# Optimization experiments

Measured on AMD Instinct MI355X. Metric: run time of the kernel, lower is better.

Reference implementation:

```python
import jax, jax.numpy as jnp
import numpy as np

T, B, NMUL = 730, 1000, 8
NEARZERO = 1e-5
LENF = 15
A_LO, A_HI = 0.1, 1.0
B_LO, B_HI = 50.0, 500.0
C_LO, C_HI = 0.0, 1.0
D_LO, D_HI = 0.01, 0.9
RA_LO, RA_HI = 0.0, 2.9
RB_LO, RB_HI = 0.0, 6.5
S_INIT, G_INIT = 50.0, 10.0


def setup_inputs() -> dict:
    key = jax.random.key(0)
    k1, k2 = jax.random.split(key)
    # forcing: prcp in [0,10) mm/day, pet in [0,5) mm/day
    x = jax.random.uniform(k1, (T, B, 2), dtype=jnp.float32) * jnp.array([10.0, 5.0], dtype=jnp.float32)
    # NN-produced raw params in [0,1): 4*NMUL physical + 2 routing
    raw_phy_static = jax.random.uniform(k2, (B, 4 * NMUL + 2), dtype=jnp.float32)
    return {"x": x, "raw_phy_static": raw_phy_static}


def _descale(p, lo, hi):
    return p * (hi - lo) + lo


def _uh_gamma(rout_a, rout_b):
    # gamma-distribution unit hydrograph, (B,) params -> (B, LENF) kernel
    aa = jax.nn.relu(rout_a)[:, None] + 0.1      # shape parameter
    theta = jax.nn.relu(rout_b)[:, None] + 0.5   # scale parameter
    t = jnp.arange(0.5, LENF, 1.0, dtype=jnp.float32)[None, :]  # midpoints 0.5..14.5
    logw = (aa - 1.0) * jnp.log(t) - t / theta - jax.scipy.special.gammaln(aa) - aa * jnp.log(theta)
    w = jnp.exp(logw)
    return w / w.sum(1, keepdims=True)


def _uh_conv(q, UH):
    # causal per-basin convolution: y[b,t] = sum_k q[b,t-k]*UH[b,k]; q (B,T), UH (B,LENF)
    n = q.shape[1]
    conv1 = lambda qb, wb: jnp.convolve(qb, wb, mode='full')[:n]
    return jax.vmap(conv1)(q, UH)


def reference(x, raw_phy_static):
    phy = raw_phy_static[:, :4 * NMUL].reshape(B, 4, NMUL)  # (B,4,NMUL)
    a = _descale(phy[:, 0], A_LO, A_HI)
    b = _descale(phy[:, 1], B_LO, B_HI)
    c = _descale(phy[:, 2], C_LO, C_HI)
    d = _descale(phy[:, 3], D_LO, D_HI)
    rout_a = _descale(raw_phy_static[:, 4 * NMUL], RA_LO, RA_HI)  # (B,)
    rout_b = _descale(raw_phy_static[:, 4 * NMUL + 1], RB_LO, RB_HI)

    ones_mul = jnp.ones((1, 1, NMUL), dtype=x.dtype)
    P = x[:, :, 0:1] * ones_mul    # (T,B,NMUL)
    PET = x[:, :, 1:2] * ones_mul  # (T,B,NMUL)

    S0 = jnp.full((B, NMUL), S_INIT, dtype=x.dtype)
    G0 = jnp.full((B, NMUL), G_INIT, dtype=x.dtype)

    def step(carry, inp):
        S, G = carry
        p, pet = inp
        W = p + S                                   # available water
        term = (W + b) / (2.0 * a)
        Y = term - jnp.sqrt(jnp.maximum(term * term - W * b / a, NEARZERO))  # ET opportunity
        S_new = Y * jnp.exp(-pet / b)               # soil storage
        AET = Y - S_new                             # actual ET
        avail = W - Y                               # water available for runoff/recharge
        Qsurf = (1.0 - c) * avail                   # direct runoff
        G_new = (G + c * avail) / (1.0 + d)         # groundwater storage
        Qgw = d * G_new                             # baseflow
        Qsim = Qsurf + Qgw
        return (S_new, G_new), (Qsim, Qsurf, Qgw, AET, S_new, G_new, W, Y)

    (_, _), (Qsim, Qsurf, Qgw, AET, Sout, Gout, Wout, Yout) = jax.lax.scan(step, (S0, G0), (P, PET))

    UH = _uh_gamma(rout_a, rout_b)                  # (B,LENF)
    Qs = _uh_conv(Qsim.mean(-1).T, UH).T[..., None]        # routed streamflow (T,B,1)
    Qsurf_r = _uh_conv(Qsurf.mean(-1).T, UH).T[..., None]  # routed surface runoff
    Qgw_r = _uh_conv(Qgw.mean(-1).T, UH).T[..., None]      # routed groundwater flow

    out = jnp.concatenate([
        Qs, Qsurf_r, Qgw_r,
        AET.mean(-1, keepdims=True),
        Sout.mean(-1, keepdims=True),
        Gout.mean(-1, keepdims=True),
    ], axis=-1)  # (T,B,6)
    return out
```

## Files before the change

kernel.cpp:

```cpp
#include <hip/hip_runtime.h>
#include <math.h>

#define T_STEPS 730
#define NB      1000
#define LENF    15
#define NEARZ   1e-5f
#define SGW     8000
#define TT      50
#define BBLK    32

#define STEPA(CURV)                                                            \
  {                                                                            \
    float pcp = (CURV).x, pet = (CURV).y;                                      \
    float W     = pcp + S;                                                     \
    float term  = fmaf(W, inv2a, pb2a);                                        \
    float disc  = fmaf(term, term, -(W * boa));                                \
    float r     = __builtin_amdgcn_sqrtf(fmaxf(disc, NEARZ));                  \
    float Y     = term - r;                                                    \
    float e     = __builtin_amdgcn_exp2f(pet * nbl);                           \
    float Sn    = Y * e;                                                       \
    float avail = W - Y;                                                       \
    float Gn    = fmaf(pc, avail, G) * i1d;                                    \
    S = Sn; G = Gn;                                                            \
    *psg = make_float2(Sn, Gn);                                                \
    psg += SGW;                                                                \
  }

#define PREFETCH(BUF, CI)                                                      \
  _Pragma("unroll")                                                            \
  for (int j = 0; j < 8; ++j) {                                                \
      BUF[j] = xs[((CI) * 8 + j) * 8 + bl];                                    \
  }                                                                            \
  __builtin_amdgcn_sched_barrier(0);

__global__ __launch_bounds__(64, 1) void scan_state(const float* __restrict__ x,
                                                    const float* __restrict__ raw,
                                                    float2* __restrict__ sg) {
    __shared__ float4 xs4[2944];
    const float2* xs = (const float2*)xs4;

    const int L   = threadIdx.x;
    const int gid = blockIdx.x * 64 + L;
    const int b   = gid >> 3;
    const int m   = gid & 7;
    const int bl  = L >> 3;

    {
        float4 tmp[46];
#pragma unroll
        for (int ch = 0; ch < 46; ++ch) {
            int idx = ch * 64 + L;
            int row = idx >> 2;
            row = row < T_STEPS ? row : (T_STEPS - 1);
            tmp[ch] = *(const float4*)((const char*)x + (size_t)row * (NB * 8)
                                       + (size_t)(blockIdx.x * 64)
                                       + (size_t)(idx & 3) * 16);
        }
#pragma unroll
        for (int ch = 0; ch < 46; ++ch) xs4[ch * 64 + L] = tmp[ch];
    }
    __syncthreads();

    const float* rp = raw + b * 34;
    float pa = rp[0 * 8 + m] * 0.9f + 0.1f;
    float pb = rp[1 * 8 + m] * 450.0f + 50.0f;
    float pc = rp[2 * 8 + m];
    float pd = rp[3 * 8 + m] * 0.89f + 0.01f;

    float inv2a = 1.0f / (2.0f * pa);
    float pb2a  = pb * inv2a;
    float boa   = pb / pa;
    float nbl   = -1.4426950408889634f / pb;
    float i1d   = 1.0f / (1.0f + pd);

    float S = 50.0f, G = 10.0f;
    float2* psg = sg + gid;

    float2 A[8], Bb[8], Cc[8];
    PREFETCH(A, 0)
    PREFETCH(Bb, 1)

    for (int g = 0; g < 15; ++g) {
        const int c0 = 6 * g;
        PREFETCH(Cc, c0 + 2)
#pragma unroll
        for (int j = 0; j < 8; ++j) STEPA(A[j])
        PREFETCH(A, c0 + 3)
#pragma unroll
        for (int j = 0; j < 8; ++j) STEPA(Bb[j])
        PREFETCH(Bb, c0 + 4)
#pragma unroll
        for (int j = 0; j < 8; ++j) STEPA(Cc[j])
        PREFETCH(Cc, c0 + 5)
#pragma unroll
        for (int j = 0; j < 8; ++j) STEPA(A[j])
        PREFETCH(A, c0 + 6)
#pragma unroll
        for (int j = 0; j < 8; ++j) STEPA(Bb[j])
        PREFETCH(Bb, c0 + 7)
#pragma unroll
        for (int j = 0; j < 8; ++j) STEPA(Cc[j])
    }
#pragma unroll
    for (int j = 0; j < 8; ++j) STEPA(A[j])
    STEPA(Bb[0])
    STEPA(Bb[1])
}

template <int CTRL>
__device__ __forceinline__ float dpp_mov(float x) {
    int xi = __builtin_bit_cast(int, x);
    int r  = __builtin_amdgcn_update_dpp(0, xi, CTRL, 0xF, 0xF, true);
    return __builtin_bit_cast(float, r);
}
__device__ __forceinline__ float sum8(float v) {
    v += dpp_mov<0xB1>(v);
    v += dpp_mov<0x4E>(v);
    v += dpp_mov<0x141>(v);
    return v;
}

__global__ __launch_bounds__(256) void finalize(const float* __restrict__ x,
                                                const float* __restrict__ raw,
                                                const float2* __restrict__ sg,
                                                float* __restrict__ out) {
    __shared__ float qsh[TT + 14][BBLK + 1];
    __shared__ float qgh[TT + 14][BBLK + 1];

    const int tid   = threadIdx.x;
    const int lb    = tid >> 3;
    const int m     = tid & 7;
    const int tbase = blockIdx.x * TT;
    const int b0    = blockIdx.y * BBLK;
    const int b     = b0 + lb;
    const bool bval = b < NB;
    const int bc    = bval ? b : (NB - 1);
    const int lane  = bc * 8 + m;

    const float* rp = raw + bc * 34;
    float pbm = rp[8 + m] * 450.0f + 50.0f;
    float e2s = 1.4426950408889634f / pbm;
    float omc = 1.0f - rp[16 + m];
    float dm  = rp[24 + m] * 0.89f + 0.01f;

    const float2* __restrict__ xf = (const float2*)x;

    float2 sgb[4], pvb[4];
#pragma unroll
    for (int d = 0; d < 4; ++d) {
        int tt = tbase + d - 14;
        int tc = tt < 0 ? 0 : (tt >= T_STEPS ? T_STEPS - 1 : tt);
        sgb[d] = sg[(size_t)tc * SGW + lane];
        pvb[d] = xf[tc * NB + bc];
    }
    float Sprev = (tbase > 0) ? sg[(size_t)(tbase - 15) * SGW + lane].x : 50.0f;

    for (int rr = 0; rr < TT + 14; rr += 4) {
#pragma unroll
        for (int d = 0; d < 4; ++d) {
            const int r  = rr + d;
            const int tt = tbase + r - 14;
            float2 sgv = sgb[d];
            float2 pv  = pvb[d];
            {
                int tn = tt + 4;
                int tc = tn < 0 ? 0 : (tn >= T_STEPS ? T_STEPS - 1 : tn);
                sgb[d] = sg[(size_t)tc * SGW + lane];
                pvb[d] = xf[tc * NB + bc];
            }
            const bool tval = (tt >= 0) && (tt < T_STEPS);
            float qs = 0.0f, qg = 0.0f, aet = 0.0f, sX = 0.0f, gX = 0.0f;
            if (tval) {
                float sp    = (tt == 0) ? 50.0f : Sprev;
                float y     = sgv.x * __builtin_amdgcn_exp2f(pv.y * e2s);
                float avail = (pv.x + sp) - y;
                qs  = omc * avail;
                qg  = dm * sgv.y;
                aet = y - sgv.x;
                sX  = sgv.x;
                gX  = sgv.y;
            }
            qs = sum8(qs);
            qg = sum8(qg);
            if (m == 0) { qsh[r][lb] = qs; qgh[r][lb] = qg; }
            if (r >= 14 && tval) {
                float a_s = sum8(aet);
                float s_s = sum8(sX);
                float g_s = sum8(gX);
                if (bval && m < 3) {
                    float v = (m == 0) ? a_s : ((m == 1) ? s_s : g_s);
                    out[((size_t)tt * NB + b) * 6 + 3 + m] = v * 0.125f;
                }
            }
            Sprev = sgv.x;
        }
    }
    __syncthreads();

    const int bl2 = tid & 31;
    const int tl0 = tid >> 5;
    const int b2  = b0 + bl2;
    if (b2 >= NB) return;

    const float* rp2 = raw + b2 * 34;
    float ra = rp2[32] * 2.9f;
    float rb = rp2[33] * 6.5f;
    float aa = fmaxf(ra, 0.0f) + 0.1f;
    float th = fmaxf(rb, 0.0f) + 0.5f;
    float inv_th = 1.0f / th;
    float am1 = aa - 1.0f;
    float w[LENF];
    float sw = 0.0f;
#pragma unroll
    for (int k = 0; k < LENF; ++k) {
        float tk = (float)k + 0.5f;
        w[k] = __expf(am1 * __logf(tk) - tk * inv_th);
        sw += w[k];
    }
    float invs = 0.125f / sw;
#pragma unroll
    for (int k = 0; k < LENF; ++k) w[k] *= invs;

#pragma unroll
    for (int it = 0; it < 7; ++it) {
        int tl = tl0 + it * 8;
        int t  = tbase + tl;
        if (tl < TT && t < T_STEPS) {
            float ys = 0.0f, yg = 0.0f;
#pragma unroll
            for (int k = 0; k < LENF; ++k) {
                ys = fmaf(qsh[tl + 14 - k][bl2], w[k], ys);
                yg = fmaf(qgh[tl + 14 - k][bl2], w[k], yg);
            }
            float* o = out + ((size_t)t * NB + b2) * 6;
            o[0] = ys + yg;
            o[1] = ys;
            o[2] = yg;
        }
    }
}

#define STEPF(CURV)                                                            \
  {                                                                            \
    float pcp = (CURV).x, pet = (CURV).y;                                      \
    float W     = pcp + S;                                                     \
    float term  = fmaf(W, inv2a, pb2a);                                        \
    float disc  = fmaf(term, term, -(W * boa));                                \
    float r     = __builtin_amdgcn_sqrtf(fmaxf(disc, NEARZ));                  \
    float Y     = term - r;                                                    \
    float e     = __builtin_amdgcn_exp2f(pet * ninvbl2);                       \
    float Sn    = Y * e;                                                       \
    float AET   = Y - Sn;                                                      \
    float avail = W - Y;                                                       \
    float Qs    = omc * avail;                                                 \
    float Gn    = fmaf(pc, avail, G) * inv1pd;                                 \
    float Qg    = pd * Gn;                                                     \
    S = Sn; G = Gn;                                                            \
    float qs_s = sum8(Qs);                                                     \
    float qg_s = sum8(Qg);                                                     \
    float ae_s = sum8(AET);                                                    \
    float s_s  = sum8(Sn);                                                     \
    float g_s  = sum8(Gn);                                                     \
    float v = qs_s;                                                            \
    v = (m == 1) ? qg_s : v;                                                   \
    v = (m == 2) ? ae_s : v;                                                   \
    v = (m == 3) ? s_s  : v;                                                   \
    v = (m >= 4) ? g_s  : v;                                                   \
    *optr = v * 0.125f;                                                        \
    optr += incr;                                                              \
  }

__global__ __launch_bounds__(64, 1) void scan_fb(const float* __restrict__ x,
                                                 const float* __restrict__ raw,
                                                 float* __restrict__ out,
                                                 float* __restrict__ qs_ws,
                                                 float* __restrict__ qg_ws,
                                                 float* __restrict__ dummy) {
    const int L  = threadIdx.x;
    const int lb = L >> 3;
    const int m  = L & 7;
    const int b  = blockIdx.x * 8 + lb;

    const float* rp = raw + b * 34;
    float pa = rp[0 * 8 + m] * 0.9f + 0.1f;
    float pb = rp[1 * 8 + m] * 450.0f + 50.0f;
    float pc = rp[2 * 8 + m];
    float pd = rp[3 * 8 + m] * 0.89f + 0.01f;
    float inv2a   = 1.0f / (2.0f * pa);
    float pb2a    = pb * inv2a;
    float boa     = pb / pa;
    float ninvbl2 = -1.4426950408889634f / pb;
    float omc     = 1.0f - pc;
    float inv1pd  = 1.0f / (1.0f + pd);

    float* optr;
    long long incr;
    if      (m == 0) { optr = qs_ws + b;                      incr = NB;     }
    else if (m == 1) { optr = qg_ws + b;                      incr = NB;     }
    else if (m <= 4) { optr = out + (long long)b * 6 + m + 1; incr = NB * 6; }
    else             { optr = dummy + (blockIdx.x * 64 + L);  incr = 0;      }

    float S = 50.0f, G = 10.0f;
    const float2* __restrict__ xf = (const float2*)x;

    float2 A[10], B[10], C[10];
#pragma unroll
    for (int j = 0; j < 10; ++j) A[j] = xf[j * NB + b];
#pragma unroll
    for (int j = 0; j < 10; ++j) B[j] = xf[(10 + j) * NB + b];

    for (int cg = 0; cg < 24; ++cg) {
        const int c0 = 3 * cg;
#pragma unroll
        for (int j = 0; j < 10; ++j) C[j] = xf[((c0 + 2) * 10 + j) * NB + b];
        __builtin_amdgcn_sched_barrier(0);
#pragma unroll
        for (int j = 0; j < 10; ++j) STEPF(A[j]);
#pragma unroll
        for (int j = 0; j < 10; ++j) A[j] = xf[((c0 + 3) * 10 + j) * NB + b];
        __builtin_amdgcn_sched_barrier(0);
#pragma unroll
        for (int j = 0; j < 10; ++j) STEPF(B[j]);
#pragma unroll
        for (int j = 0; j < 10; ++j) {
            int t = (c0 + 4) * 10 + j;
            t = t < T_STEPS ? t : (T_STEPS - 1);
            B[j] = xf[t * NB + b];
        }
        __builtin_amdgcn_sched_barrier(0);
#pragma unroll
        for (int j = 0; j < 10; ++j) STEPF(C[j]);
    }
#pragma unroll
    for (int j = 0; j < 10; ++j) STEPF(A[j]);
}

__global__ __launch_bounds__(256) void uh_fb(const float* __restrict__ raw,
                                             float* __restrict__ uh) {
    int b = blockIdx.x * 256 + threadIdx.x;
    if (b >= NB) return;
    float ra = raw[b * 34 + 32] * 2.9f;
    float rb = raw[b * 34 + 33] * 6.5f;
    float aa = fmaxf(ra, 0.0f) + 0.1f;
    float th = fmaxf(rb, 0.0f) + 0.5f;
    float inv_th = 1.0f / th;
    float am1 = aa - 1.0f;
    float w[LENF];
    float s = 0.0f;
#pragma unroll
    for (int k = 0; k < LENF; ++k) {
        float t = (float)k + 0.5f;
        w[k] = __expf(am1 * __logf(t) - t * inv_th);
        s += w[k];
    }
    float invs = 1.0f / s;
#pragma unroll
    for (int k = 0; k < LENF; ++k) uh[k * NB + b] = w[k] * invs;
}

__global__ __launch_bounds__(256) void conv_fb(const float* __restrict__ qs_ws,
                                               const float* __restrict__ qg_ws,
                                               const float* __restrict__ uh,
                                               float* __restrict__ out) {
    int b = blockIdx.x * 256 + threadIdx.x;
    int t = blockIdx.y;
    if (b >= NB) return;
    float ys = 0.0f, yg = 0.0f;
    int kmax = t < (LENF - 1) ? t : (LENF - 1);
    for (int k = 0; k <= kmax; ++k) {
        float w = uh[k * NB + b];
        ys = fmaf(qs_ws[(t - k) * NB + b], w, ys);
        yg = fmaf(qg_ws[(t - k) * NB + b], w, yg);
    }
    float* o = out + (t * NB + b) * 6;
    o[0] = ys + yg;
    o[1] = ys;
    o[2] = yg;
}

extern "C" void kernel_launch(void* const* d_in, const int* in_sizes, int n_in,
                              void* d_out, int out_size, void* d_ws, size_t ws_size,
                              hipStream_t stream) {
    const float* x   = (const float*)d_in[0];
    const float* raw = (const float*)d_in[1];
    float* out = (float*)d_out;

    const size_t need = (size_t)T_STEPS * SGW * sizeof(float2);
    if (ws_size >= need) {
        float2* sg = (float2*)d_ws;
        scan_state<<<dim3(SGW / 64), dim3(64),  0, stream>>>(x, raw, sg);
        finalize  <<<dim3((T_STEPS + TT - 1) / TT, (NB + BBLK - 1) / BBLK),
                     dim3(256), 0, stream>>>(x, raw, sg, out);
    } else {
        float* qs = (float*)d_ws;
        float* qg = qs + (size_t)T_STEPS * NB;
        float* uh = qg + (size_t)T_STEPS * NB;
        float* dm = uh + (size_t)LENF * NB;
        uh_fb  <<<dim3((NB + 255) / 256),          dim3(256), 0, stream>>>(raw, uh);
        scan_fb<<<dim3(NB / 8),                    dim3(64),  0, stream>>>(x, raw, out, qs, qg, dm);
        conv_fb<<<dim3((NB + 255) / 256, T_STEPS), dim3(256), 0, stream>>>(qs, qg, uh, out);
    }
}
```

Measured before the change: 113.6 us.

## Fuse member-mean reductions into scan and split routing into separate UH and conv kernels

The scan kernel now computes Qsurf, Qgw, AET, S and G in place and reduces them across the 8 multipliers with DPP lane shuffles. It writes the per-basin mean flows and state outputs directly, so the full per-member S/G state is no longer written to the workspace and re-read. A small kernel builds the unit hydrograph, and a separate conv kernel does the causal convolution from the reduced (T,B) flow buffer. This cuts workspace traffic roughly eightfold. In exchange, the latency-bound serial scan carries five DPP reductions and strided global stores per step, and it adds a third kernel launch.

```diff
diff --git a/kernel.cpp b/kernel.cpp
--- a/kernel.cpp
+++ b/kernel.cpp
@@ -6,24 +6,44 @@
 #define LENF    15
 #define NEARZ   1e-5f
 #define SGW     8000
-#define TT      50
-#define BBLK    32
-
-#define STEPA(CURV)                                                            \
-  {                                                                            \
-    float pcp = (CURV).x, pet = (CURV).y;                                      \
-    float W     = pcp + S;                                                     \
-    float term  = fmaf(W, inv2a, pb2a);                                        \
-    float disc  = fmaf(term, term, -(W * boa));                                \
-    float r     = __builtin_amdgcn_sqrtf(fmaxf(disc, NEARZ));                  \
-    float Y     = term - r;                                                    \
-    float e     = __builtin_amdgcn_exp2f(pet * nbl);                           \
-    float Sn    = Y * e;                                                       \
-    float avail = W - Y;                                                       \
-    float Gn    = fmaf(pc, avail, G) * i1d;                                    \
-    S = Sn; G = Gn;                                                            \
-    *psg = make_float2(Sn, Gn);                                                \
-    psg += SGW;                                                                \
+
+template <int CTRL>
+__device__ __forceinline__ float dpp_mov(float x) {
+    int xi = __builtin_bit_cast(int, x);
+    int r  = __builtin_amdgcn_update_dpp(0, xi, CTRL, 0xF, 0xF, true);
+    return __builtin_bit_cast(float, r);
+}
+__device__ __forceinline__ float sum8(float v) {
+    v += dpp_mov<0xB1>(v);
+    v += dpp_mov<0x4E>(v);
+    v += dpp_mov<0x141>(v);
+    return v;
+}
+
+#define STEPC(CURV)                                                           \
+  {                                                                           \
+    float pcp = (CURV).x, pet = (CURV).y;                                     \
+    float W     = pcp + S;                                                    \
+    float term  = fmaf(W, inv2a, pb2a);                                       \
+    float disc  = fmaf(term, term, -(W * boa));                               \
+    float r     = __builtin_amdgcn_sqrtf(fmaxf(disc, NEARZ));                 \
+    float Y     = term - r;                                                   \
+    float e     = __builtin_amdgcn_exp2f(pet * nbl);                          \
+    float Sn    = Y * e;                                                      \
+    float avail = W - Y;                                                      \
+    float Gn    = fmaf(pc, avail, G) * i1d;                                   \
+    float Qs    = omc * avail;                                                \
+    float Qg    = pd * Gn;                                                    \
+    S = Sn; G = Gn;                                                           \
+    float qs_s = sum8(Qs);                                                    \
+    float qg_s = sum8(Qg);                                                    \
+    float y_s  = sum8(Y);                                                     \
+    float s_s  = sum8(Sn);                                                    \
+    float g_s  = sum8(Gn);                                                    \
+    if (m == 3) *qp = make_float2(qs_s, qg_s);                                \
+    float ov = (m == 0) ? (y_s - s_s) : ((m == 1) ? s_s : g_s);               \
+    if (m < 3) *optr = ov * 0.125f;                                           \
+    qp += NB; optr += NB * 6;                                                 \
   }
 
 #define PREFETCH(BUF, CI)                                                      \
@@ -33,9 +53,10 @@
   }                                                                            \
   __builtin_amdgcn_sched_barrier(0);
 
-__global__ __launch_bounds__(64, 1) void scan_state(const float* __restrict__ x,
+__global__ __launch_bounds__(64, 1) void scan_fused(const float* __restrict__ x,
                                                     const float* __restrict__ raw,
-                                                    float2* __restrict__ sg) {
+                                                    float2* __restrict__ qsg,
+                                                    float* __restrict__ out) {
     __shared__ float4 xs4[2944];
     const float2* xs = (const float2*)xs4;
 
@@ -72,9 +93,11 @@
     float boa   = pb / pa;
     float nbl   = -1.4426950408889634f / pb;
     float i1d   = 1.0f / (1.0f + pd);
+    float omc   = 1.0f - pc;
 
     float S = 50.0f, G = 10.0f;
-    float2* psg = sg + gid;
+    float2* qp   = qsg + b;
+    float*  optr = out + (size_t)b * 6 + 3 + (m < 3 ? m : 0);
 
     float2 A[8], Bb[8], Cc[8];
     PREFETCH(A, 0)
@@ -84,160 +107,69 @@
         const int c0 = 6 * g;
         PREFETCH(Cc, c0 + 2)
 #pragma unroll
-        for (int j = 0; j < 8; ++j) STEPA(A[j])
+        for (int j = 0; j < 8; ++j) STEPC(A[j])
         PREFETCH(A, c0 + 3)
 #pragma unroll
-        for (int j = 0; j < 8; ++j) STEPA(Bb[j])
+        for (int j = 0; j < 8; ++j) STEPC(Bb[j])
         PREFETCH(Bb, c0 + 4)
 #pragma unroll
-        for (int j = 0; j < 8; ++j) STEPA(Cc[j])
+        for (int j = 0; j < 8; ++j) STEPC(Cc[j])
         PREFETCH(Cc, c0 + 5)
 #pragma unroll
-        for (int j = 0; j < 8; ++j) STEPA(A[j])
+        for (int j = 0; j < 8; ++j) STEPC(A[j])
         PREFETCH(A, c0 + 6)
 #pragma unroll
-        for (int j = 0; j < 8; ++j) STEPA(Bb[j])
+        for (int j = 0; j < 8; ++j) STEPC(Bb[j])
         PREFETCH(Bb, c0 + 7)
 #pragma unroll
-        for (int j = 0; j < 8; ++j) STEPA(Cc[j])
-    }
-#pragma unroll
-    for (int j = 0; j < 8; ++j) STEPA(A[j])
-    STEPA(Bb[0])
-    STEPA(Bb[1])
-}
-
-template <int CTRL>
-__device__ __forceinline__ float dpp_mov(float x) {
-    int xi = __builtin_bit_cast(int, x);
-    int r  = __builtin_amdgcn_update_dpp(0, xi, CTRL, 0xF, 0xF, true);
-    return __builtin_bit_cast(float, r);
-}
-__device__ __forceinline__ float sum8(float v) {
-    v += dpp_mov<0xB1>(v);
-    v += dpp_mov<0x4E>(v);
-    v += dpp_mov<0x141>(v);
-    return v;
-}
-
-__global__ __launch_bounds__(256) void finalize(const float* __restrict__ x,
-                                                const float* __restrict__ raw,
-                                                const float2* __restrict__ sg,
-                                                float* __restrict__ out) {
-    __shared__ float qsh[TT + 14][BBLK + 1];
-    __shared__ float qgh[TT + 14][BBLK + 1];
-
-    const int tid   = threadIdx.x;
-    const int lb    = tid >> 3;
-    const int m     = tid & 7;
-    const int tbase = blockIdx.x * TT;
-    const int b0    = blockIdx.y * BBLK;
-    const int b     = b0 + lb;
-    const bool bval = b < NB;
-    const int bc    = bval ? b : (NB - 1);
-    const int lane  = bc * 8 + m;
-
-    const float* rp = raw + bc * 34;
-    float pbm = rp[8 + m] * 450.0f + 50.0f;
-    float e2s = 1.4426950408889634f / pbm;
-    float omc = 1.0f - rp[16 + m];
-    float dm  = rp[24 + m] * 0.89f + 0.01f;
-
-    const float2* __restrict__ xf = (const float2*)x;
-
-    float2 sgb[4], pvb[4];
-#pragma unroll
-    for (int d = 0; d < 4; ++d) {
-        int tt = tbase + d - 14;
-        int tc = tt < 0 ? 0 : (tt >= T_STEPS ? T_STEPS - 1 : tt);
-        sgb[d] = sg[(size_t)tc * SGW + lane];
-        pvb[d] = xf[tc * NB + bc];
-    }
-    float Sprev = (tbase > 0) ? sg[(size_t)(tbase - 15) * SGW + lane].x : 50.0f;
-
-    for (int rr = 0; rr < TT + 14; rr += 4) {
-#pragma unroll
-        for (int d = 0; d < 4; ++d) {
-            const int r  = rr + d;
-            const int tt = tbase + r - 14;
-            float2 sgv = sgb[d];
-            float2 pv  = pvb[d];
-            {
-                int tn = tt + 4;
-                int tc = tn < 0 ? 0 : (tn >= T_STEPS ? T_STEPS - 1 : tn);
-                sgb[d] = sg[(size_t)tc * SGW + lane];
-                pvb[d] = xf[tc * NB + bc];
-            }
-            const bool tval = (tt >= 0) && (tt < T_STEPS);
-            float qs = 0.0f, qg = 0.0f, aet = 0.0f, sX = 0.0f, gX = 0.0f;
-            if (tval) {
-                float sp    = (tt == 0) ? 50.0f : Sprev;
-                float y     = sgv.x * __builtin_amdgcn_exp2f(pv.y * e2s);
-                float avail = (pv.x + sp) - y;
-                qs  = omc * avail;
-                qg  = dm * sgv.y;
-                aet = y - sgv.x;
-                sX  = sgv.x;
-                gX  = sgv.y;
-            }
-            qs = sum8(qs);
-            qg = sum8(qg);
-            if (m == 0) { qsh[r][lb] = qs; qgh[r][lb] = qg; }
-            if (r >= 14 && tval) {
-                float a_s = sum8(aet);
-                float s_s = sum8(sX);
-                float g_s = sum8(gX);
-                if (bval && m < 3) {
-                    float v = (m == 0) ? a_s : ((m == 1) ? s_s : g_s);
-                    out[((size_t)tt * NB + b) * 6 + 3 + m] = v * 0.125f;
-                }
-            }
-            Sprev = sgv.x;
-        }
-    }
-    __syncthreads();
-
-    const int bl2 = tid & 31;
-    const int tl0 = tid >> 5;
-    const int b2  = b0 + bl2;
-    if (b2 >= NB) return;
-
-    const float* rp2 = raw + b2 * 34;
-    float ra = rp2[32] * 2.9f;
-    float rb = rp2[33] * 6.5f;
+        for (int j = 0; j < 8; ++j) STEPC(Cc[j])
+    }
+#pragma unroll
+    for (int j = 0; j < 8; ++j) STEPC(A[j])
+    STEPC(Bb[0])
+    STEPC(Bb[1])
+}
+
+__global__ __launch_bounds__(256) void uh_k(const float* __restrict__ raw,
+                                            float* __restrict__ uh) {
+    int b = blockIdx.x * 256 + threadIdx.x;
+    if (b >= NB) return;
+    float ra = raw[b * 34 + 32] * 2.9f;
+    float rb = raw[b * 34 + 33] * 6.5f;
     float aa = fmaxf(ra, 0.0f) + 0.1f;
     float th = fmaxf(rb, 0.0f) + 0.5f;
     float inv_th = 1.0f / th;
     float am1 = aa - 1.0f;
     float w[LENF];
-    float sw = 0.0f;
+    float s = 0.0f;
 #pragma unroll
     for (int k = 0; k < LENF; ++k) {
-        float tk = (float)k + 0.5f;
-        w[k] = __expf(am1 * __logf(tk) - tk * inv_th);
-        sw += w[k];
-    }
-    float invs = 0.125f / sw;
-#pragma unroll
-    for (int k = 0; k < LENF; ++k) w[k] *= invs;
-
-#pragma unroll
-    for (int it = 0; it < 7; ++it) {
-        int tl = tl0 + it * 8;
-        int t  = tbase + tl;
-        if (tl < TT && t < T_STEPS) {
-            float ys = 0.0f, yg = 0.0f;
-#pragma unroll
-            for (int k = 0; k < LENF; ++k) {
-                ys = fmaf(qsh[tl + 14 - k][bl2], w[k], ys);
-                yg = fmaf(qgh[tl + 14 - k][bl2], w[k], yg);
-            }
-            float* o = out + ((size_t)t * NB + b2) * 6;
-            o[0] = ys + yg;
-            o[1] = ys;
-            o[2] = yg;
-        }
-    }
+        float t = (float)k + 0.5f;
+        w[k] = __expf(am1 * __logf(t) - t * inv_th);
+        s += w[k];
+    }
+    float invs = 0.125f / s;
+#pragma unroll
+    for (int k = 0; k < LENF; ++k) uh[k * NB + b] = w[k] * invs;
+}
+
+__global__ __launch_bounds__(256) void conv2(const float2* __restrict__ qsg,
+                                             const float* __restrict__ uh,
+                                             float* __restrict__ out) {
+    int b = blockIdx.x * 256 + threadIdx.x;
+    int t = blockIdx.y;
+    if (b >= NB) return;
+    float ys = 0.0f, yg = 0.0f;
+    int kmax = t < (LENF - 1) ? t : (LENF - 1);
+    for (int k = 0; k <= kmax; ++k) {
+        float w  = uh[k * NB + b];
+        float2 q = qsg[(size_t)(t - k) * NB + b];
+        ys = fmaf(q.x, w, ys);
+        yg = fmaf(q.y, w, yg);
+    }
+    float* o = out + ((size_t)t * NB + b) * 6;
+    *(float2*)o = make_float2(ys + yg, ys);
+    o[2] = yg;
 }
 
 #define STEPF(CURV)                                                            \
@@ -385,12 +317,14 @@
     const float* raw = (const float*)d_in[1];
     float* out = (float*)d_out;
 
-    const size_t need = (size_t)T_STEPS * SGW * sizeof(float2);
+    const size_t need = (size_t)T_STEPS * NB * sizeof(float2)
+                      + (size_t)LENF * NB * sizeof(float);
     if (ws_size >= need) {
-        float2* sg = (float2*)d_ws;
-        scan_state<<<dim3(SGW / 64), dim3(64),  0, stream>>>(x, raw, sg);
-        finalize  <<<dim3((T_STEPS + TT - 1) / TT, (NB + BBLK - 1) / BBLK),
-                     dim3(256), 0, stream>>>(x, raw, sg, out);
+        float2* qsg = (float2*)d_ws;
+        float*  uh  = (float*)(qsg + (size_t)T_STEPS * NB);
+        uh_k      <<<dim3((NB + 255) / 256), dim3(256), 0, stream>>>(raw, uh);
+        scan_fused<<<dim3(SGW / 64),         dim3(64),  0, stream>>>(x, raw, qsg, out);
+        conv2     <<<dim3((NB + 255) / 256, T_STEPS), dim3(256), 0, stream>>>(qsg, uh, out);
     } else {
         float* qs = (float*)d_ws;
         float* qg = qs + (size_t)T_STEPS * NB;
```

New measurement: 216.3 us. 1.9x slower.

## Store only S per step with sparse G checkpoints, recompute G in finalize

Applied to the files above, without the earlier changes.

The scan kernel now writes only the soil storage S for each step, packing two steps per float2, and writes groundwater G only at checkpoints spaced one finalize tile apart. The finalize kernel reloads G from the checkpoint and recomputes the G recurrence across its tile, including the 14-step halo. The time tile grows from 50 to 64 to match the checkpoint spacing. This roughly halves workspace write and read traffic in exchange for a serial G recurrence in finalize and extra per-step bookkeeping in the scan.

```diff
diff --git a/kernel.cpp b/kernel.cpp
--- a/kernel.cpp
+++ b/kernel.cpp
@@ -6,10 +6,26 @@
 #define LENF    15
 #define NEARZ   1e-5f
 #define SGW     8000
-#define TT      50
+#define TT      64
 #define BBLK    32
-
-#define STEPA(CURV)                                                            \
+#define NPAIR   365
+#define NCHK    11
+
+
+template <int CTRL>
+__device__ __forceinline__ float dpp_mov(float x) {
+    int xi = __builtin_bit_cast(int, x);
+    int r  = __builtin_amdgcn_update_dpp(0, xi, CTRL, 0xF, 0xF, true);
+    return __builtin_bit_cast(float, r);
+}
+__device__ __forceinline__ float sum8(float v) {
+    v += dpp_mov<0xB1>(v);
+    v += dpp_mov<0x4E>(v);
+    v += dpp_mov<0x141>(v);
+    return v;
+}
+
+#define STEPA(CURV, TB, J)                                                     \
   {                                                                            \
     float pcp = (CURV).x, pet = (CURV).y;                                      \
     float W     = pcp + S;                                                     \
@@ -22,8 +38,9 @@
     float avail = W - Y;                                                       \
     float Gn    = fmaf(pc, avail, G) * i1d;                                    \
     S = Sn; G = Gn;                                                            \
-    *psg = make_float2(Sn, Gn);                                                \
-    psg += SGW;                                                                \
+    if (((J) & 1) == 0) Skeep = Sn;                                            \
+    else { *ps2 = make_float2(Skeep, Sn); ps2 += SGW; }                        \
+    if ((TB) + (J) == nextchk) { *gc = Gn; gc += SGW; nextchk += TT; }         \
   }
 
 #define PREFETCH(BUF, CI)                                                      \
@@ -35,7 +52,8 @@
 
 __global__ __launch_bounds__(64, 1) void scan_state(const float* __restrict__ x,
                                                     const float* __restrict__ raw,
-                                                    float2* __restrict__ sg) {
+                                                    float2* __restrict__ sp,
+                                                    float* __restrict__ gchk) {
     __shared__ float4 xs4[2944];
     const float2* xs = (const float2*)xs4;
 
@@ -73,8 +91,10 @@
     float nbl   = -1.4426950408889634f / pb;
     float i1d   = 1.0f / (1.0f + pd);
 
-    float S = 50.0f, G = 10.0f;
-    float2* psg = sg + gid;
+    float S = 50.0f, G = 10.0f, Skeep = 0.0f;
+    float2* ps2 = sp + gid;
+    float*  gc  = gchk + gid;
+    int nextchk = TT - 15;
 
     float2 A[8], Bb[8], Cc[8];
     PREFETCH(A, 0)
@@ -82,47 +102,76 @@
 
     for (int g = 0; g < 15; ++g) {
         const int c0 = 6 * g;
+        const int t0 = 48 * g;
         PREFETCH(Cc, c0 + 2)
 #pragma unroll
-        for (int j = 0; j < 8; ++j) STEPA(A[j])
+        for (int j = 0; j < 8; ++j) STEPA(A[j],  t0,      j)
         PREFETCH(A, c0 + 3)
 #pragma unroll
-        for (int j = 0; j < 8; ++j) STEPA(Bb[j])
+        for (int j = 0; j < 8; ++j) STEPA(Bb[j], t0 + 8,  j)
         PREFETCH(Bb, c0 + 4)
 #pragma unroll
-        for (int j = 0; j < 8; ++j) STEPA(Cc[j])
+        for (int j = 0; j < 8; ++j) STEPA(Cc[j], t0 + 16, j)
         PREFETCH(Cc, c0 + 5)
 #pragma unroll
-        for (int j = 0; j < 8; ++j) STEPA(A[j])
+        for (int j = 0; j < 8; ++j) STEPA(A[j],  t0 + 24, j)
         PREFETCH(A, c0 + 6)
 #pragma unroll
-        for (int j = 0; j < 8; ++j) STEPA(Bb[j])
+        for (int j = 0; j < 8; ++j) STEPA(Bb[j], t0 + 32, j)
         PREFETCH(Bb, c0 + 7)
 #pragma unroll
-        for (int j = 0; j < 8; ++j) STEPA(Cc[j])
-    }
-#pragma unroll
-    for (int j = 0; j < 8; ++j) STEPA(A[j])
-    STEPA(Bb[0])
-    STEPA(Bb[1])
-}
-
-template <int CTRL>
-__device__ __forceinline__ float dpp_mov(float x) {
-    int xi = __builtin_bit_cast(int, x);
-    int r  = __builtin_amdgcn_update_dpp(0, xi, CTRL, 0xF, 0xF, true);
-    return __builtin_bit_cast(float, r);
-}
-__device__ __forceinline__ float sum8(float v) {
-    v += dpp_mov<0xB1>(v);
-    v += dpp_mov<0x4E>(v);
-    v += dpp_mov<0x141>(v);
-    return v;
-}
+        for (int j = 0; j < 8; ++j) STEPA(Cc[j], t0 + 40, j)
+    }
+#pragma unroll
+    for (int j = 0; j < 8; ++j) STEPA(A[j], 720, j)
+    STEPA(Bb[0], 728, 0)
+    STEPA(Bb[1], 728, 1)
+}
+
+#define ROW(SN, XV, TTE, RE)                                                   \
+  {                                                                            \
+    const int tt = (TTE); const int r = (RE);                                  \
+    const bool tval = (tt >= 0) && (tt < T_STEPS);                             \
+    float qs = 0.f, qg = 0.f, aet = 0.f, sX = 0.f, gX = 0.f;                   \
+    if (tval) {                                                                \
+      float sn  = (SN);                                                        \
+      float spv = (tt == 0) ? 50.0f : Sprev;                                   \
+      float y   = sn * __builtin_amdgcn_exp2f((XV).y * e2s);                   \
+      float avail = ((XV).x + spv) - y;                                        \
+      G = fmaf(pc, avail, G) * i1d;                                            \
+      qs = omc * avail; qg = pd * G; aet = y - sn; sX = sn; gX = G;            \
+      Sprev = sn;                                                              \
+    }                                                                          \
+    qs = sum8(qs); qg = sum8(qg);                                              \
+    if (m == 0) { qsh[r][lb] = qs; qgh[r][lb] = qg; }                          \
+    if (r >= 14 && tval) {                                                     \
+      float a_s = sum8(aet), s_s = sum8(sX), g_s = sum8(gX);                   \
+      if (bval && m < 3) {                                                     \
+        float v = (m == 0) ? a_s : ((m == 1) ? s_s : g_s);                     \
+        out[((size_t)tt * NB + b) * 6 + 3 + m] = v * 0.125f;                   \
+      }                                                                        \
+    }                                                                          \
+  }
+
+#define PAIRSTEP(PH)                                                           \
+  {                                                                            \
+    const int pidx = g2 * 3 + (PH);                                            \
+    const int tt0  = tbase - 14 + 2 * pidx;                                    \
+    float2 sv  = sb[PH];                                                       \
+    float2 xv0 = x0b[PH];                                                      \
+    float2 xv1 = x1b[PH];                                                      \
+    { int tp = tt0 + 6; tp = tp < 0 ? 0 : (tp > 728 ? 728 : tp);               \
+      sb[PH]  = sp[(size_t)(tp >> 1) * SGW + lane];                            \
+      x0b[PH] = xf[tp * NB + bc];                                              \
+      x1b[PH] = xf[(tp + 1) * NB + bc]; }                                      \
+    ROW(sv.x, xv0, tt0,     2 * pidx)                                          \
+    ROW(sv.y, xv1, tt0 + 1, 2 * pidx + 1)                                      \
+  }
 
 __global__ __launch_bounds__(256) void finalize(const float* __restrict__ x,
                                                 const float* __restrict__ raw,
-                                                const float2* __restrict__ sg,
+                                                const float2* __restrict__ sp,
+                                                const float* __restrict__ gchk,
                                                 float* __restrict__ out) {
     __shared__ float qsh[TT + 14][BBLK + 1];
     __shared__ float qgh[TT + 14][BBLK + 1];
@@ -140,60 +189,32 @@
     const float* rp = raw + bc * 34;
     float pbm = rp[8 + m] * 450.0f + 50.0f;
     float e2s = 1.4426950408889634f / pbm;
-    float omc = 1.0f - rp[16 + m];
-    float dm  = rp[24 + m] * 0.89f + 0.01f;
+    float pc  = rp[16 + m];
+    float omc = 1.0f - pc;
+    float pd  = rp[24 + m] * 0.89f + 0.01f;
+    float i1d = 1.0f / (1.0f + pd);
 
     const float2* __restrict__ xf = (const float2*)x;
 
-    float2 sgb[4], pvb[4];
-#pragma unroll
-    for (int d = 0; d < 4; ++d) {
-        int tt = tbase + d - 14;
-        int tc = tt < 0 ? 0 : (tt >= T_STEPS ? T_STEPS - 1 : tt);
-        sgb[d] = sg[(size_t)tc * SGW + lane];
-        pvb[d] = xf[tc * NB + bc];
-    }
-    float Sprev = (tbase > 0) ? sg[(size_t)(tbase - 15) * SGW + lane].x : 50.0f;
-
-    for (int rr = 0; rr < TT + 14; rr += 4) {
-#pragma unroll
-        for (int d = 0; d < 4; ++d) {
-            const int r  = rr + d;
-            const int tt = tbase + r - 14;
-            float2 sgv = sgb[d];
-            float2 pv  = pvb[d];
-            {
-                int tn = tt + 4;
-                int tc = tn < 0 ? 0 : (tn >= T_STEPS ? T_STEPS - 1 : tn);
-                sgb[d] = sg[(size_t)tc * SGW + lane];
-                pvb[d] = xf[tc * NB + bc];
-            }
-            const bool tval = (tt >= 0) && (tt < T_STEPS);
-            float qs = 0.0f, qg = 0.0f, aet = 0.0f, sX = 0.0f, gX = 0.0f;
-            if (tval) {
-                float sp    = (tt == 0) ? 50.0f : Sprev;
-                float y     = sgv.x * __builtin_amdgcn_exp2f(pv.y * e2s);
-                float avail = (pv.x + sp) - y;
-                qs  = omc * avail;
-                qg  = dm * sgv.y;
-                aet = y - sgv.x;
-                sX  = sgv.x;
-                gX  = sgv.y;
-            }
-            qs = sum8(qs);
-            qg = sum8(qg);
-            if (m == 0) { qsh[r][lb] = qs; qgh[r][lb] = qg; }
-            if (r >= 14 && tval) {
-                float a_s = sum8(aet);
-                float s_s = sum8(sX);
-                float g_s = sum8(gX);
-                if (bval && m < 3) {
-                    float v = (m == 0) ? a_s : ((m == 1) ? s_s : g_s);
-                    out[((size_t)tt * NB + b) * 6 + 3 + m] = v * 0.125f;
-                }
-            }
-            Sprev = sgv.x;
-        }
+    float G     = (blockIdx.x == 0) ? 10.0f
+                  : gchk[(size_t)(blockIdx.x - 1) * SGW + lane];
+    float Sprev = 50.0f;
+    if (tbase > 0) Sprev = sp[(size_t)((tbase - 16) >> 1) * SGW + lane].y;
+
+    float2 sb[3], x0b[3], x1b[3];
+#pragma unroll
+    for (int d = 0; d < 3; ++d) {
+        int tp = tbase - 14 + 2 * d;
+        tp = tp < 0 ? 0 : (tp > 728 ? 728 : tp);
+        sb[d]  = sp[(size_t)(tp >> 1) * SGW + lane];
+        x0b[d] = xf[tp * NB + bc];
+        x1b[d] = xf[(tp + 1) * NB + bc];
+    }
+
+    for (int g2 = 0; g2 < 13; ++g2) {
+        PAIRSTEP(0)
+        PAIRSTEP(1)
+        PAIRSTEP(2)
     }
     __syncthreads();
 
@@ -222,10 +243,10 @@
     for (int k = 0; k < LENF; ++k) w[k] *= invs;
 
 #pragma unroll
-    for (int it = 0; it < 7; ++it) {
+    for (int it = 0; it < 8; ++it) {
         int tl = tl0 + it * 8;
         int t  = tbase + tl;
-        if (tl < TT && t < T_STEPS) {
+        if (t < T_STEPS) {
             float ys = 0.0f, yg = 0.0f;
 #pragma unroll
             for (int k = 0; k < LENF; ++k) {
@@ -385,12 +406,14 @@
     const float* raw = (const float*)d_in[1];
     float* out = (float*)d_out;
 
-    const size_t need = (size_t)T_STEPS * SGW * sizeof(float2);
+    const size_t need = (size_t)NPAIR * SGW * sizeof(float2)
+                      + (size_t)NCHK * SGW * sizeof(float);
     if (ws_size >= need) {
-        float2* sg = (float2*)d_ws;
-        scan_state<<<dim3(SGW / 64), dim3(64),  0, stream>>>(x, raw, sg);
+        float2* sp   = (float2*)d_ws;
+        float*  gchk = (float*)(sp + (size_t)NPAIR * SGW);
+        scan_state<<<dim3(SGW / 64), dim3(64),  0, stream>>>(x, raw, sp, gchk);
         finalize  <<<dim3((T_STEPS + TT - 1) / TT, (NB + BBLK - 1) / BBLK),
-                     dim3(256), 0, stream>>>(x, raw, sg, out);
+                     dim3(256), 0, stream>>>(x, raw, sp, gchk, out);
     } else {
         float* qs = (float*)d_ws;
         float* qg = qs + (size_t)T_STEPS * NB;
```

Measured after the change: 125.9 us. 1.11x slower.

## Interleave two independent basin recurrences per thread in the state scan

Applied to the files above, without the earlier changes.

Each thread of the scan kernel now advances two independent basin/multiplier chains (basins 8 apart) instead of one, halving the block count to 63 and doubling the shared-memory forcing tile. Interleaving the two dependent sqrt/fma chains is meant to hide the latency of the serial recurrence, since only one wave runs per block. The PET exponential is also moved out of the step into the prefetch stage. The state buffer stride grows to 8064 to fit the padded layout, and the finalize kernel is updated to match. The cost is more registers and fewer waves across the GPU.

```diff
diff --git a/kernel.cpp b/kernel.cpp
--- a/kernel.cpp
+++ b/kernel.cpp
@@ -5,106 +5,129 @@
 #define NB      1000
 #define LENF    15
 #define NEARZ   1e-5f
-#define SGW     8000
+#define SGW2    8064
 #define TT      50
 #define BBLK    32
 
-#define STEPA(CURV)                                                            \
+#define STEP2(V0, V1)                                                          \
   {                                                                            \
-    float pcp = (CURV).x, pet = (CURV).y;                                      \
-    float W     = pcp + S;                                                     \
-    float term  = fmaf(W, inv2a, pb2a);                                        \
-    float disc  = fmaf(term, term, -(W * boa));                                \
-    float r     = __builtin_amdgcn_sqrtf(fmaxf(disc, NEARZ));                  \
-    float Y     = term - r;                                                    \
-    float e     = __builtin_amdgcn_exp2f(pet * nbl);                           \
-    float Sn    = Y * e;                                                       \
-    float avail = W - Y;                                                       \
-    float Gn    = fmaf(pc, avail, G) * i1d;                                    \
-    S = Sn; G = Gn;                                                            \
-    *psg = make_float2(Sn, Gn);                                                \
-    psg += SGW;                                                                \
+    float W0  = (V0).x + S0;                                                   \
+    float t0  = fmaf(W0, inv2a0, pb2a0);                                       \
+    float d0  = fmaf(t0, t0, -(W0 * boa0));                                    \
+    float r0  = __builtin_amdgcn_sqrtf(fmaxf(d0, NEARZ));                      \
+    float Y0  = t0 - r0;                                                       \
+    float Sn0 = Y0 * (V0).y;                                                   \
+    float av0 = W0 - Y0;                                                       \
+    float Gn0 = fmaf(pc0, av0, G0) * i1d0;                                     \
+    float W1  = (V1).x + S1;                                                   \
+    float t1  = fmaf(W1, inv2a1, pb2a1);                                       \
+    float d1  = fmaf(t1, t1, -(W1 * boa1));                                    \
+    float r1  = __builtin_amdgcn_sqrtf(fmaxf(d1, NEARZ));                      \
+    float Y1  = t1 - r1;                                                       \
+    float Sn1 = Y1 * (V1).y;                                                   \
+    float av1 = W1 - Y1;                                                       \
+    float Gn1 = fmaf(pc1, av1, G1) * i1d1;                                     \
+    S0 = Sn0; G0 = Gn0; S1 = Sn1; G1 = Gn1;                                    \
+    ps0[0]  = make_float2(Sn0, Gn0);                                           \
+    ps0[64] = make_float2(Sn1, Gn1);                                           \
+    ps0 += SGW2;                                                               \
   }
 
-#define PREFETCH(BUF, CI)                                                      \
+#define PREFETCH(B0, B1, CI)                                                   \
   _Pragma("unroll")                                                            \
   for (int j = 0; j < 8; ++j) {                                                \
-      BUF[j] = xs[((CI) * 8 + j) * 8 + bl];                                    \
+      float2 v0 = xs[((CI) * 8 + j) * 16 + bl0];                               \
+      float2 v1 = xs[((CI) * 8 + j) * 16 + bl1];                               \
+      B0[j] = make_float2(v0.x, __builtin_amdgcn_exp2f(v0.y * nbl0));          \
+      B1[j] = make_float2(v1.x, __builtin_amdgcn_exp2f(v1.y * nbl1));          \
   }                                                                            \
   __builtin_amdgcn_sched_barrier(0);
 
 __global__ __launch_bounds__(64, 1) void scan_state(const float* __restrict__ x,
                                                     const float* __restrict__ raw,
                                                     float2* __restrict__ sg) {
-    __shared__ float4 xs4[2944];
+    __shared__ float4 xs4[5888];
     const float2* xs = (const float2*)xs4;
 
     const int L   = threadIdx.x;
-    const int gid = blockIdx.x * 64 + L;
-    const int b   = gid >> 3;
-    const int m   = gid & 7;
-    const int bl  = L >> 3;
-
-    {
-        float4 tmp[46];
-#pragma unroll
-        for (int ch = 0; ch < 46; ++ch) {
-            int idx = ch * 64 + L;
-            int row = idx >> 2;
+    const int blk = blockIdx.x;
+    const int bl0 = L >> 3;
+    const int bl1 = bl0 + 8;
+    const int m   = L & 7;
+    int b0 = blk * 16 + bl0; if (b0 > NB - 1) b0 = NB - 1;
+    int b1 = blk * 16 + 8 + bl0; if (b1 > NB - 1) b1 = NB - 1;
+
+    for (int rd = 0; rd < 4; ++rd) {
+        float4 tmp[23];
+#pragma unroll
+        for (int ch = 0; ch < 23; ++ch) {
+            int idx = (rd * 23 + ch) * 64 + L;
+            int row = idx >> 3;
+            int col = idx & 7;
             row = row < T_STEPS ? row : (T_STEPS - 1);
-            tmp[ch] = *(const float4*)((const char*)x + (size_t)row * (NB * 8)
-                                       + (size_t)(blockIdx.x * 64)
-                                       + (size_t)(idx & 3) * 16);
+            int bo = blk * 128 + col * 16;
+            bo = bo <= 8000 - 16 ? bo : 8000 - 16;
+            tmp[ch] = *(const float4*)((const char*)x + (size_t)row * (NB * 8) + bo);
         }
 #pragma unroll
-        for (int ch = 0; ch < 46; ++ch) xs4[ch * 64 + L] = tmp[ch];
+        for (int ch = 0; ch < 23; ++ch) xs4[(rd * 23 + ch) * 64 + L] = tmp[ch];
     }
     __syncthreads();
 
-    const float* rp = raw + b * 34;
-    float pa = rp[0 * 8 + m] * 0.9f + 0.1f;
-    float pb = rp[1 * 8 + m] * 450.0f + 50.0f;
-    float pc = rp[2 * 8 + m];
-    float pd = rp[3 * 8 + m] * 0.89f + 0.01f;
-
-    float inv2a = 1.0f / (2.0f * pa);
-    float pb2a  = pb * inv2a;
-    float boa   = pb / pa;
-    float nbl   = -1.4426950408889634f / pb;
-    float i1d   = 1.0f / (1.0f + pd);
-
-    float S = 50.0f, G = 10.0f;
-    float2* psg = sg + gid;
-
-    float2 A[8], Bb[8], Cc[8];
-    PREFETCH(A, 0)
-    PREFETCH(Bb, 1)
+    const float* rp0 = raw + b0 * 34;
+    const float* rp1 = raw + b1 * 34;
+    float pa0 = rp0[0 * 8 + m] * 0.9f + 0.1f;
+    float pb0 = rp0[1 * 8 + m] * 450.0f + 50.0f;
+    float pc0 = rp0[2 * 8 + m];
+    float pd0 = rp0[3 * 8 + m] * 0.89f + 0.01f;
+    float pa1 = rp1[0 * 8 + m] * 0.9f + 0.1f;
+    float pb1 = rp1[1 * 8 + m] * 450.0f + 50.0f;
+    float pc1 = rp1[2 * 8 + m];
+    float pd1 = rp1[3 * 8 + m] * 0.89f + 0.01f;
+
+    float inv2a0 = 1.0f / (2.0f * pa0);
+    float pb2a0  = pb0 * inv2a0;
+    float boa0   = pb0 / pa0;
+    float nbl0   = -1.4426950408889634f / pb0;
+    float i1d0   = 1.0f / (1.0f + pd0);
+    float inv2a1 = 1.0f / (2.0f * pa1);
+    float pb2a1  = pb1 * inv2a1;
+    float boa1   = pb1 / pa1;
+    float nbl1   = -1.4426950408889634f / pb1;
+    float i1d1   = 1.0f / (1.0f + pd1);
+
+    float S0 = 50.0f, G0 = 10.0f, S1 = 50.0f, G1 = 10.0f;
+    float2* ps0 = sg + blk * 128 + L;
+
+    float2 A0[8], A1[8], B0[8], B1[8], C0[8], C1[8];
+    PREFETCH(A0, A1, 0)
+    PREFETCH(B0, B1, 1)
 
     for (int g = 0; g < 15; ++g) {
         const int c0 = 6 * g;
-        PREFETCH(Cc, c0 + 2)
-#pragma unroll
-        for (int j = 0; j < 8; ++j) STEPA(A[j])
-        PREFETCH(A, c0 + 3)
-#pragma unroll
-        for (int j = 0; j < 8; ++j) STEPA(Bb[j])
-        PREFETCH(Bb, c0 + 4)
-#pragma unroll
-        for (int j = 0; j < 8; ++j) STEPA(Cc[j])
-        PREFETCH(Cc, c0 + 5)
-#pragma unroll
-        for (int j = 0; j < 8; ++j) STEPA(A[j])
-        PREFETCH(A, c0 + 6)
-#pragma unroll
-        for (int j = 0; j < 8; ++j) STEPA(Bb[j])
-        PREFETCH(Bb, c0 + 7)
-#pragma unroll
-        for (int j = 0; j < 8; ++j) STEPA(Cc[j])
-    }
-#pragma unroll
-    for (int j = 0; j < 8; ++j) STEPA(A[j])
-    STEPA(Bb[0])
-    STEPA(Bb[1])
+        PREFETCH(C0, C1, c0 + 2)
+#pragma unroll
+        for (int j = 0; j < 8; ++j) STEP2(A0[j], A1[j])
+        PREFETCH(A0, A1, c0 + 3)
+#pragma unroll
+        for (int j = 0; j < 8; ++j) STEP2(B0[j], B1[j])
+        PREFETCH(B0, B1, c0 + 4)
+#pragma unroll
+        for (int j = 0; j < 8; ++j) STEP2(C0[j], C1[j])
+        PREFETCH(C0, C1, c0 + 5)
+#pragma unroll
+        for (int j = 0; j < 8; ++j) STEP2(A0[j], A1[j])
+        PREFETCH(A0, A1, c0 + 6)
+#pragma unroll
+        for (int j = 0; j < 8; ++j) STEP2(B0[j], B1[j])
+        PREFETCH(B0, B1, c0 + 7)
+#pragma unroll
+        for (int j = 0; j < 8; ++j) STEP2(C0[j], C1[j])
+    }
+#pragma unroll
+    for (int j = 0; j < 8; ++j) STEP2(A0[j], A1[j])
+    STEP2(B0[0], B1[0])
+    STEP2(B0[1], B1[1])
 }
 
 template <int CTRL>
@@ -150,10 +173,10 @@
     for (int d = 0; d < 4; ++d) {
         int tt = tbase + d - 14;
         int tc = tt < 0 ? 0 : (tt >= T_STEPS ? T_STEPS - 1 : tt);
-        sgb[d] = sg[(size_t)tc * SGW + lane];
+        sgb[d] = sg[(size_t)tc * SGW2 + lane];
         pvb[d] = xf[tc * NB + bc];
     }
-    float Sprev = (tbase > 0) ? sg[(size_t)(tbase - 15) * SGW + lane].x : 50.0f;
+    float Sprev = (tbase > 0) ? sg[(size_t)(tbase - 15) * SGW2 + lane].x : 50.0f;
 
     for (int rr = 0; rr < TT + 14; rr += 4) {
 #pragma unroll
@@ -165,7 +188,7 @@
             {
                 int tn = tt + 4;
                 int tc = tn < 0 ? 0 : (tn >= T_STEPS ? T_STEPS - 1 : tn);
-                sgb[d] = sg[(size_t)tc * SGW + lane];
+                sgb[d] = sg[(size_t)tc * SGW2 + lane];
                 pvb[d] = xf[tc * NB + bc];
             }
             const bool tval = (tt >= 0) && (tt < T_STEPS);
@@ -385,10 +408,10 @@
     const float* raw = (const float*)d_in[1];
     float* out = (float*)d_out;
 
-    const size_t need = (size_t)T_STEPS * SGW * sizeof(float2);
+    const size_t need = (size_t)T_STEPS * SGW2 * sizeof(float2);
     if (ws_size >= need) {
         float2* sg = (float2*)d_ws;
-        scan_state<<<dim3(SGW / 64), dim3(64),  0, stream>>>(x, raw, sg);
+        scan_state<<<dim3(63), dim3(64),  0, stream>>>(x, raw, sg);
         finalize  <<<dim3((T_STEPS + TT - 1) / TT, (NB + BBLK - 1) / BBLK),
                      dim3(256), 0, stream>>>(x, raw, sg, out);
     } else {
```

Result: slower. 141.4 us (+24.5%).
